# Performance work log

Measured on AMD Instinct MI355X. Metric: run time of the kernel, lower is better.

The kernel has to match this reference:

```python
import jax, jax.numpy as jnp
import numpy as np

B_SIZE, STEPS, UNITS = 128, 1024, 1024
E = 2 * STEPS              # model_internal_dim = expand_factor * model_input_dims
DT_RANK = (STEPS + 1) // 2 # math.ceil(model_input_dims / 2)
N = UNITS // 2             # model_states
COND = 512                 # conditioning feature size
K = 4                      # conv kernel size


def setup_inputs() -> dict:
    key = jax.random.key(0)
    ks = jax.random.split(key, 12)
    s = lambda k, shape, fan: jax.random.normal(k, shape, jnp.float32) / np.sqrt(fan)
    return {
        "x": jax.random.normal(ks[0], (B_SIZE, 1, STEPS), jnp.float32),
        "c": jax.random.normal(ks[1], (B_SIZE, COND), jnp.float32),
        "ln_g": jnp.ones((STEPS,), jnp.float32),
        "ln_b": jnp.zeros((STEPS,), jnp.float32),
        "W_in": s(ks[2], (STEPS, 2 * E), STEPS),
        "conv_w": s(ks[3], (K, 1, E), K),
        "conv_b": jnp.zeros((E,), jnp.float32),
        "W_x": s(ks[4], (E, DT_RANK + 2 * N), E),
        "W_dt": s(ks[5], (DT_RANK, E), DT_RANK),
        "b_dt": jnp.zeros((E,), jnp.float32),
        "A_log": jnp.log(jnp.tile(jnp.arange(1, N + 1, dtype=jnp.float32), (E, 1))),
        "D": jnp.ones((E,), jnp.float32),
        "W_out": s(ks[6], (E, STEPS), E),
        "b_out": jnp.zeros((STEPS,), jnp.float32),
        "W_d": s(ks[7], (STEPS, N), STEPS),
        "b_d": jnp.zeros((N,), jnp.float32),
        "W_f": s(ks[8], (COND, 2 * N), COND),
        "b_f": jnp.zeros((2 * N,), jnp.float32),
        "W_o": s(ks[9], (N, STEPS), N),
        "b_o": jnp.zeros((STEPS,), jnp.float32),
    }


def _selective_scan(u, delta, A, Bm, Cm, D):
    # u, delta: (b,l,e); A: (e,n); Bm, Cm: (b,l,n); D: (e,)
    dA = jnp.exp(jnp.einsum('ble,en->blen', delta, A))        # discretized A
    dBu = jnp.einsum('ble,ble,bln->blen', delta, u, Bm)       # discretized B*u

    def step(h, t):
        dA_t, dBu_t, C_t = t
        h = dA_t * h + dBu_t                                  # (b,e,n)
        return h, jnp.einsum('ben,bn->be', h, C_t)

    h0 = jnp.zeros((dA.shape[0], dA.shape[2], dA.shape[3]), dA.dtype)
    _, ys = jax.lax.scan(step, h0, (dA.transpose(1, 0, 2, 3),
                                    dBu.transpose(1, 0, 2, 3),
                                    Cm.transpose(1, 0, 2)))
    y = ys.transpose(1, 0, 2)                                 # (b,l,e)
    return y + u * D


def reference(x, c, ln_g, ln_b, W_in, conv_w, conv_b, W_x, W_dt, b_dt,
              A_log, D, W_out, b_out, W_d, b_d, W_f, b_f, W_o, b_o):
    # --- ResidualBlock: LayerNorm -> MambaBlock -> + x ---
    mu = jnp.mean(x, -1, keepdims=True)
    var = jnp.var(x, -1, keepdims=True)
    h = (x - mu) * jax.lax.rsqrt(var + 1e-5) * ln_g + ln_b
    xz = h @ W_in                                             # (b,l,2E)
    xi, res = jnp.split(xz, 2, axis=-1)
    xc = jax.lax.conv_general_dilated(
        xi, conv_w, window_strides=(1,), padding=[(K - 1, 0)],
        dimension_numbers=('NWC', 'WIO', 'NWC'), feature_group_count=E) + conv_b
    u = jax.nn.silu(xc)
    x_dbl = u @ W_x                                           # (b,l,dt_rank+2N)
    d_r, Bm, Cm = jnp.split(x_dbl, [DT_RANK, DT_RANK + N], axis=-1)
    delta = jax.nn.softplus(d_r @ W_dt + b_dt)                # (b,l,E)
    A = -jnp.exp(A_log)
    y = _selective_scan(u, delta, A, Bm, Cm, D)
    y = y * jax.nn.silu(res)                                  # gating branch
    mamba_out = y @ W_out + b_out + x                         # residual add
    # --- Dense(model_states, gelu) then squeeze seq dim ---
    z = jax.nn.gelu(mamba_out @ W_d + b_d, approximate=False)
    z = jnp.squeeze(z, axis=1)                                # (b, N)
    # --- FiLM conditioning ---
    gb = c @ W_f + b_f
    g, b = jnp.split(gb, 2, axis=-1)
    z = z * g + b
    # --- output projection back to steps ---
    return z @ W_o + b_o
```

## Files before the change

### kernel.cpp

```cpp
#include <hip/hip_runtime.h>
#include <math.h>

#define E_DIM 2048

typedef __attribute__((ext_vector_type(8))) short short8;
typedef __attribute__((ext_vector_type(4))) float floatx4;

__device__ __forceinline__ float siluf(float v) { return v / (1.f + expf(-v)); }

__device__ __forceinline__ short f2bf(float f) {
    unsigned u = __float_as_uint(f);
    u += 0x7fffu + ((u >> 16) & 1u);
    return (short)(u >> 16);
}

__global__ __launch_bounds__(256) void ln_cvt_kernel(const float* __restrict__ x,
                                                     const float* __restrict__ g,
                                                     const float* __restrict__ be,
                                                     const float* __restrict__ c,
                                                     short* __restrict__ h_bf,
                                                     short* __restrict__ c_bf) {
    int b = blockIdx.x;
    int tid = threadIdx.x;
    __shared__ float sdata[256];
    const float* xr = x + b * 1024;
    float v[4];
    float s = 0.f;
#pragma unroll
    for (int i = 0; i < 4; ++i) { v[i] = xr[tid + i * 256]; s += v[i]; }
    sdata[tid] = s; __syncthreads();
    for (int st = 128; st > 0; st >>= 1) { if (tid < st) sdata[tid] += sdata[tid + st]; __syncthreads(); }
    float mu = sdata[0] * (1.f / 1024.f);
    __syncthreads();
    float s2 = 0.f;
#pragma unroll
    for (int i = 0; i < 4; ++i) { float d = v[i] - mu; s2 += d * d; }
    sdata[tid] = s2; __syncthreads();
    for (int st = 128; st > 0; st >>= 1) { if (tid < st) sdata[tid] += sdata[tid + st]; __syncthreads(); }
    float var = sdata[0] * (1.f / 1024.f);
    float inv = rsqrtf(var + 1e-5f);
    short* hr = h_bf + b * 1024;
#pragma unroll
    for (int i = 0; i < 4; ++i) {
        int j = tid + i * 256;
        hr[j] = f2bf((v[i] - mu) * inv * g[j] + be[j]);
    }
    const float* cr = c + b * 512;
    short* cbr = c_bf + b * 512;
    for (int j = tid; j < 512; j += 256) cbr[j] = f2bf(cr[j]);
}

__global__ __launch_bounds__(256) void gemm_mfma(const short* __restrict__ A, int lda,
                                                 const float* __restrict__ B, int ldb,
                                                 float* __restrict__ C, int ldc,
                                                 int kChunk) {
    const int tid = threadIdx.x;
    const int w = tid >> 6;
    const int l = tid & 63;
    const int lane15 = l & 15;
    const int lgrp = l >> 4;
    const int n0 = blockIdx.x * 64;
    const int k0 = blockIdx.z * kChunk;

    const short* Ap0 = A + (w * 32 + lane15) * lda + lgrp * 8 + k0;
    const short* Ap1 = Ap0 + 16 * lda;
    const float* Bp = B + (size_t)(k0 + lgrp * 8) * ldb + n0 + lane15;

    floatx4 acc[2][4];
#pragma unroll
    for (int i = 0; i < 2; ++i)
#pragma unroll
        for (int j = 0; j < 4; ++j) acc[i][j] = (floatx4)0.f;

    for (int ks = 0; ks < kChunk; ks += 32) {
        short8 a0 = *(const short8*)(Ap0);
        short8 a1 = *(const short8*)(Ap1);
        Ap0 += 32; Ap1 += 32;
        float bv[4][8];
#pragma unroll
        for (int i = 0; i < 8; ++i) {
            const float* Br = Bp + i * ldb;
#pragma unroll
            for (int nt = 0; nt < 4; ++nt) bv[nt][i] = Br[nt * 16];
        }
        Bp += 32 * (size_t)ldb;
        short8 vb[4];
#pragma unroll
        for (int nt = 0; nt < 4; ++nt)
#pragma unroll
            for (int i = 0; i < 8; ++i) vb[nt][i] = f2bf(bv[nt][i]);
#pragma unroll
        for (int nt = 0; nt < 4; ++nt) {
            acc[0][nt] = __builtin_amdgcn_mfma_f32_16x16x32_bf16(a0, vb[nt], acc[0][nt], 0, 0, 0);
            acc[1][nt] = __builtin_amdgcn_mfma_f32_16x16x32_bf16(a1, vb[nt], acc[1][nt], 0, 0, 0);
        }
    }
    const int rbase = w * 32 + lgrp * 4;
#pragma unroll
    for (int mf = 0; mf < 2; ++mf)
#pragma unroll
        for (int nt = 0; nt < 4; ++nt)
#pragma unroll
            for (int r = 0; r < 4; ++r)
                atomicAdd(&C[(rbase + mf * 16 + r) * ldc + n0 + nt * 16 + lane15], acc[mf][nt][r]);
}

__global__ __launch_bounds__(256) void e1_kernel(const float* __restrict__ xz,
                                                 const float* __restrict__ convw,
                                                 const float* __restrict__ convb,
                                                 float* __restrict__ u_f32,
                                                 short* __restrict__ u_bf,
                                                 float* __restrict__ sres) {
    int idx = blockIdx.x * 256 + threadIdx.x;
    int b = idx >> 12, j = idx & 4095;
    float val = xz[idx];
    if (j < E_DIM) {
        float xc = val * convw[3 * E_DIM + j] + convb[j];
        float s = siluf(xc);
        u_f32[b * E_DIM + j] = s;
        u_bf[b * E_DIM + j] = f2bf(s);
    } else {
        sres[b * E_DIM + (j - E_DIM)] = siluf(val);
    }
}

__global__ __launch_bounds__(256) void svec_cvt_kernel(const float* __restrict__ xdbl,
                                                       float* __restrict__ svec,
                                                       short* __restrict__ dr_bf) {
    int b = blockIdx.x;
    int tid = threadIdx.x;
    __shared__ float sdata[256];
    const float* row = xdbl + b * 1536;
    float s = 0.f;
    for (int n = tid; n < 512; n += 256) s += row[512 + n] * row[1024 + n];
    sdata[tid] = s; __syncthreads();
    for (int st = 128; st > 0; st >>= 1) { if (tid < st) sdata[tid] += sdata[tid + st]; __syncthreads(); }
    if (tid == 0) svec[b] = sdata[0];
    short* dr = dr_bf + b * 512;
    for (int n = tid; n < 512; n += 256) dr[n] = f2bf(row[n]);
}

__global__ __launch_bounds__(256) void e3_kernel(const float* __restrict__ dacc,
                                                 const float* __restrict__ b_dt,
                                                 const float* __restrict__ u,
                                                 const float* __restrict__ sres,
                                                 const float* __restrict__ svec,
                                                 const float* __restrict__ Dv,
                                                 short* __restrict__ y_bf) {
    int idx = blockIdx.x * 256 + threadIdx.x;
    int b = idx >> 11, j = idx & 2047;
    float t = dacc[idx] + b_dt[j];
    float delta = fmaxf(t, 0.f) + log1pf(expf(-fabsf(t)));
    y_bf[idx] = f2bf(u[idx] * (delta * svec[b] + Dv[j]) * sres[idx]);
}

__global__ __launch_bounds__(256) void e4_kernel(const float* __restrict__ mo,
                                                 const float* __restrict__ b_out,
                                                 const float* __restrict__ x,
                                                 short* __restrict__ mamba_bf) {
    int idx = blockIdx.x * 256 + threadIdx.x;
    int j = idx & 1023;
    mamba_bf[idx] = f2bf(mo[idx] + b_out[j] + x[idx]);
}

__global__ __launch_bounds__(256) void e5_kernel(const float* __restrict__ zd,
                                                 const float* __restrict__ b_d,
                                                 const float* __restrict__ gb,
                                                 const float* __restrict__ b_f,
                                                 short* __restrict__ z_bf) {
    int idx = blockIdx.x * 256 + threadIdx.x;
    int b = idx >> 9, n = idx & 511;
    float t = zd[idx] + b_d[n];
    float zg = 0.5f * t * (1.f + erff(t * 0.70710678118654752f));
    float gq = gb[b * 1024 + n] + b_f[n];
    float bb = gb[b * 1024 + 512 + n] + b_f[512 + n];
    z_bf[idx] = f2bf(zg * gq + bb);
}

__global__ __launch_bounds__(256) void e6_kernel(const float* __restrict__ oa,
                                                 const float* __restrict__ b_o,
                                                 float* __restrict__ out) {
    int idx = blockIdx.x * 256 + threadIdx.x;
    int j = idx & 1023;
    out[idx] = oa[idx] + b_o[j];
}

extern "C" void kernel_launch(void* const* d_in, const int* in_sizes, int n_in,
                              void* d_out, int out_size, void* d_ws, size_t ws_size,
                              hipStream_t stream) {
    (void)in_sizes; (void)n_in; (void)out_size; (void)ws_size;
    const float* x     = (const float*)d_in[0];
    const float* c     = (const float*)d_in[1];
    const float* ln_g  = (const float*)d_in[2];
    const float* ln_b  = (const float*)d_in[3];
    const float* W_in  = (const float*)d_in[4];
    const float* convw = (const float*)d_in[5];
    const float* convb = (const float*)d_in[6];
    const float* W_x   = (const float*)d_in[7];
    const float* W_dt  = (const float*)d_in[8];
    const float* b_dt  = (const float*)d_in[9];
    const float* Dv    = (const float*)d_in[11];
    const float* W_out = (const float*)d_in[12];
    const float* b_out = (const float*)d_in[13];
    const float* W_d   = (const float*)d_in[14];
    const float* b_d   = (const float*)d_in[15];
    const float* W_f   = (const float*)d_in[16];
    const float* b_f   = (const float*)d_in[17];
    const float* W_o   = (const float*)d_in[18];
    const float* b_o   = (const float*)d_in[19];
    float* out = (float*)d_out;

    char* ws = (char*)d_ws;
    size_t off = 0;
    auto allocf = [&](size_t nElem) { float* p = (float*)(ws + off); off += nElem * sizeof(float); return p; };
    auto allocs = [&](size_t nElem) { short* p = (short*)(ws + off); off += nElem * sizeof(short); return p; };
    float* xz_acc   = allocf(128 * 4096);
    float* xdbl_acc = allocf(128 * 1536);
    float* dacc     = allocf(128 * 2048);
    float* mo_acc   = allocf(128 * 1024);
    float* zd_acc   = allocf(128 * 512);
    float* gb_acc   = allocf(128 * 1024);
    float* out_acc  = allocf(128 * 1024);
    size_t accBytes = off;
    float* u_f32  = allocf(128 * 2048);
    float* sres   = allocf(128 * 2048);
    float* svec   = allocf(128);
    short* h_bf   = allocs(128 * 1024);
    short* c_bf   = allocs(128 * 512);
    short* u_bf   = allocs(128 * 2048);
    short* dr_bf  = allocs(128 * 512);
    short* y_bf   = allocs(128 * 2048);
    short* mamba_bf = allocs(128 * 1024);
    short* z_bf   = allocs(128 * 512);

    hipMemsetAsync(d_ws, 0, accBytes, stream);

    ln_cvt_kernel<<<128, 256, 0, stream>>>(x, ln_g, ln_b, c, h_bf, c_bf);
    gemm_mfma<<<dim3(64, 1, 4), 256, 0, stream>>>(h_bf, 1024, W_in, 4096, xz_acc, 4096, 256);
    gemm_mfma<<<dim3(16, 1, 8), 256, 0, stream>>>(c_bf, 512, W_f, 1024, gb_acc, 1024, 64);
    e1_kernel<<<(128 * 4096) / 256, 256, 0, stream>>>(xz_acc, convw, convb, u_f32, u_bf, sres);
    gemm_mfma<<<dim3(24, 1, 8), 256, 0, stream>>>(u_bf, 2048, W_x, 1536, xdbl_acc, 1536, 256);
    svec_cvt_kernel<<<128, 256, 0, stream>>>(xdbl_acc, svec, dr_bf);
    gemm_mfma<<<dim3(32, 1, 8), 256, 0, stream>>>(dr_bf, 512, W_dt, 2048, dacc, 2048, 64);
    e3_kernel<<<(128 * 2048) / 256, 256, 0, stream>>>(dacc, b_dt, u_f32, sres, svec, Dv, y_bf);
    gemm_mfma<<<dim3(16, 1, 8), 256, 0, stream>>>(y_bf, 2048, W_out, 1024, mo_acc, 1024, 256);
    e4_kernel<<<(128 * 1024) / 256, 256, 0, stream>>>(mo_acc, b_out, x, mamba_bf);
    gemm_mfma<<<dim3(8, 1, 16), 256, 0, stream>>>(mamba_bf, 1024, W_d, 512, zd_acc, 512, 64);
    e5_kernel<<<(128 * 512) / 256, 256, 0, stream>>>(zd_acc, b_d, gb_acc, b_f, z_bf);
    gemm_mfma<<<dim3(16, 1, 8), 256, 0, stream>>>(z_bf, 512, W_o, 1024, out_acc, 1024, 64);
    e6_kernel<<<(128 * 1024) / 256, 256, 0, stream>>>(out_acc, b_o, out);
}
```

Baseline: 91.39 us.

## Fuse elementwise epilogues into GEMM A-loads and merge workspace zeroing into layernorm

Removes the separate elementwise kernels (conv+silu, dr conversion, residual add, gelu+FiLM) by templating the GEMM A-fragment load so it reads fp32 accumulators and applies the transform before converting to bf16. The svec reduction and the y computation are merged into one per-row kernel that recomputes u and silu(res) directly from xz. The hipMemsetAsync is replaced by extra blocks in the layernorm kernel that zero the accumulators. This cuts launches and intermediate buffers, but A-operand loads become scalar fp32 with repeated transcendental work, since every column block recomputes the same activations.

```diff
diff --git a/kernel.cpp b/kernel.cpp
--- a/kernel.cpp
+++ b/kernel.cpp
@@ -14,43 +14,97 @@
     return (short)(u >> 16);
 }
 
-__global__ __launch_bounds__(256) void ln_cvt_kernel(const float* __restrict__ x,
-                                                     const float* __restrict__ g,
-                                                     const float* __restrict__ be,
-                                                     const float* __restrict__ c,
-                                                     short* __restrict__ h_bf,
-                                                     short* __restrict__ c_bf) {
-    int b = blockIdx.x;
+__global__ __launch_bounds__(256) void ln_zero_kernel(const float* __restrict__ x,
+                                                      const float* __restrict__ g,
+                                                      const float* __restrict__ be,
+                                                      const float* __restrict__ c,
+                                                      short* __restrict__ h_bf,
+                                                      short* __restrict__ c_bf,
+                                                      float4* __restrict__ zbase,
+                                                      int zTotal) {
     int tid = threadIdx.x;
-    __shared__ float sdata[256];
-    const float* xr = x + b * 1024;
-    float v[4];
-    float s = 0.f;
-#pragma unroll
-    for (int i = 0; i < 4; ++i) { v[i] = xr[tid + i * 256]; s += v[i]; }
-    sdata[tid] = s; __syncthreads();
-    for (int st = 128; st > 0; st >>= 1) { if (tid < st) sdata[tid] += sdata[tid + st]; __syncthreads(); }
-    float mu = sdata[0] * (1.f / 1024.f);
-    __syncthreads();
-    float s2 = 0.f;
-#pragma unroll
-    for (int i = 0; i < 4; ++i) { float d = v[i] - mu; s2 += d * d; }
-    sdata[tid] = s2; __syncthreads();
-    for (int st = 128; st > 0; st >>= 1) { if (tid < st) sdata[tid] += sdata[tid + st]; __syncthreads(); }
-    float var = sdata[0] * (1.f / 1024.f);
-    float inv = rsqrtf(var + 1e-5f);
-    short* hr = h_bf + b * 1024;
-#pragma unroll
-    for (int i = 0; i < 4; ++i) {
-        int j = tid + i * 256;
-        hr[j] = f2bf((v[i] - mu) * inv * g[j] + be[j]);
-    }
-    const float* cr = c + b * 512;
-    short* cbr = c_bf + b * 512;
-    for (int j = tid; j < 512; j += 256) cbr[j] = f2bf(cr[j]);
-}
-
-__global__ __launch_bounds__(256) void gemm_mfma(const short* __restrict__ A, int lda,
+    if (blockIdx.x < 128) {
+        int b = blockIdx.x;
+        __shared__ float sdata[256];
+        const float* xr = x + b * 1024;
+        float v[4];
+        float s = 0.f;
+#pragma unroll
+        for (int i = 0; i < 4; ++i) { v[i] = xr[tid + i * 256]; s += v[i]; }
+        sdata[tid] = s; __syncthreads();
+        for (int st = 128; st > 0; st >>= 1) { if (tid < st) sdata[tid] += sdata[tid + st]; __syncthreads(); }
+        float mu = sdata[0] * (1.f / 1024.f);
+        __syncthreads();
+        float s2 = 0.f;
+#pragma unroll
+        for (int i = 0; i < 4; ++i) { float d = v[i] - mu; s2 += d * d; }
+        sdata[tid] = s2; __syncthreads();
+        for (int st = 128; st > 0; st >>= 1) { if (tid < st) sdata[tid] += sdata[tid + st]; __syncthreads(); }
+        float var = sdata[0] * (1.f / 1024.f);
+        float inv = rsqrtf(var + 1e-5f);
+        short* hr = h_bf + b * 1024;
+#pragma unroll
+        for (int i = 0; i < 4; ++i) {
+            int j = tid + i * 256;
+            hr[j] = f2bf((v[i] - mu) * inv * g[j] + be[j]);
+        }
+        const float* cr = c + b * 512;
+        short* cbr = c_bf + b * 512;
+        for (int j = tid; j < 512; j += 256) cbr[j] = f2bf(cr[j]);
+    } else {
+        int base = (blockIdx.x - 128) * 2048 + tid;
+        int stride = (gridDim.x - 128) * 2048;
+        for (int idx = base; idx < zTotal; idx += stride) {
+#pragma unroll
+            for (int i = 0; i < 8; ++i) {
+                int k = idx + i * 256;
+                if (k < zTotal) zbase[k] = (float4){0.f, 0.f, 0.f, 0.f};
+            }
+        }
+    }
+}
+
+template<int MODE>
+__device__ __forceinline__ short8 load_a_frag(const void* __restrict__ A, int lda, int r, int j0,
+                                              const float* __restrict__ aux0,
+                                              const float* __restrict__ aux1,
+                                              const float* __restrict__ aux2) {
+    if constexpr (MODE == 0) {
+        return *(const short8*)((const short*)A + (size_t)r * lda + j0);
+    } else {
+        const float* p = (const float*)A + (size_t)r * lda + j0;
+        float v[8];
+        if constexpr (MODE == 1) {
+#pragma unroll
+            for (int i = 0; i < 8; ++i) v[i] = siluf(p[i] * aux0[j0 + i] + aux1[j0 + i]);
+        } else if constexpr (MODE == 2) {
+#pragma unroll
+            for (int i = 0; i < 8; ++i) v[i] = p[i];
+        } else if constexpr (MODE == 3) {
+#pragma unroll
+            for (int i = 0; i < 8; ++i) v[i] = p[i] + aux0[j0 + i] + aux1[(size_t)r * lda + j0 + i];
+        } else {
+#pragma unroll
+            for (int i = 0; i < 8; ++i) {
+                float t = p[i] + aux0[j0 + i];
+                float zg = 0.5f * t * (1.f + erff(t * 0.70710678118654752f));
+                float gq = aux1[(size_t)r * 1024 + j0 + i] + aux2[j0 + i];
+                float bb = aux1[(size_t)r * 1024 + 512 + j0 + i] + aux2[512 + j0 + i];
+                v[i] = zg * gq + bb;
+            }
+        }
+        short8 s;
+#pragma unroll
+        for (int i = 0; i < 8; ++i) s[i] = f2bf(v[i]);
+        return s;
+    }
+}
+
+template<int MODE>
+__global__ __launch_bounds__(256) void gemm_mfma(const void* __restrict__ A, int lda,
+                                                 const float* __restrict__ aux0,
+                                                 const float* __restrict__ aux1,
+                                                 const float* __restrict__ aux2,
                                                  const float* __restrict__ B, int ldb,
                                                  float* __restrict__ C, int ldc,
                                                  int kChunk) {
@@ -62,8 +116,7 @@
     const int n0 = blockIdx.x * 64;
     const int k0 = blockIdx.z * kChunk;
 
-    const short* Ap0 = A + (w * 32 + lane15) * lda + lgrp * 8 + k0;
-    const short* Ap1 = Ap0 + 16 * lda;
+    const int r0 = w * 32 + lane15;
     const float* Bp = B + (size_t)(k0 + lgrp * 8) * ldb + n0 + lane15;
 
     floatx4 acc[2][4];
@@ -73,9 +126,9 @@
         for (int j = 0; j < 4; ++j) acc[i][j] = (floatx4)0.f;
 
     for (int ks = 0; ks < kChunk; ks += 32) {
-        short8 a0 = *(const short8*)(Ap0);
-        short8 a1 = *(const short8*)(Ap1);
-        Ap0 += 32; Ap1 += 32;
+        int j0 = k0 + ks + lgrp * 8;
+        short8 a0 = load_a_frag<MODE>(A, lda, r0, j0, aux0, aux1, aux2);
+        short8 a1 = load_a_frag<MODE>(A, lda, r0 + 16, j0, aux0, aux1, aux2);
         float bv[4][8];
 #pragma unroll
         for (int i = 0; i < 8; ++i) {
@@ -105,28 +158,14 @@
                 atomicAdd(&C[(rbase + mf * 16 + r) * ldc + n0 + nt * 16 + lane15], acc[mf][nt][r]);
 }
 
-__global__ __launch_bounds__(256) void e1_kernel(const float* __restrict__ xz,
-                                                 const float* __restrict__ convw,
+__global__ __launch_bounds__(256) void e3_kernel(const float* __restrict__ dacc,
+                                                 const float* __restrict__ b_dt,
+                                                 const float* __restrict__ xz,
+                                                 const float* __restrict__ convw3,
                                                  const float* __restrict__ convb,
-                                                 float* __restrict__ u_f32,
-                                                 short* __restrict__ u_bf,
-                                                 float* __restrict__ sres) {
-    int idx = blockIdx.x * 256 + threadIdx.x;
-    int b = idx >> 12, j = idx & 4095;
-    float val = xz[idx];
-    if (j < E_DIM) {
-        float xc = val * convw[3 * E_DIM + j] + convb[j];
-        float s = siluf(xc);
-        u_f32[b * E_DIM + j] = s;
-        u_bf[b * E_DIM + j] = f2bf(s);
-    } else {
-        sres[b * E_DIM + (j - E_DIM)] = siluf(val);
-    }
-}
-
-__global__ __launch_bounds__(256) void svec_cvt_kernel(const float* __restrict__ xdbl,
-                                                       float* __restrict__ svec,
-                                                       short* __restrict__ dr_bf) {
+                                                 const float* __restrict__ xdbl,
+                                                 const float* __restrict__ Dv,
+                                                 short* __restrict__ y_bf) {
     int b = blockIdx.x;
     int tid = threadIdx.x;
     __shared__ float sdata[256];
@@ -135,46 +174,19 @@
     for (int n = tid; n < 512; n += 256) s += row[512 + n] * row[1024 + n];
     sdata[tid] = s; __syncthreads();
     for (int st = 128; st > 0; st >>= 1) { if (tid < st) sdata[tid] += sdata[tid + st]; __syncthreads(); }
-    if (tid == 0) svec[b] = sdata[0];
-    short* dr = dr_bf + b * 512;
-    for (int n = tid; n < 512; n += 256) dr[n] = f2bf(row[n]);
-}
-
-__global__ __launch_bounds__(256) void e3_kernel(const float* __restrict__ dacc,
-                                                 const float* __restrict__ b_dt,
-                                                 const float* __restrict__ u,
-                                                 const float* __restrict__ sres,
-                                                 const float* __restrict__ svec,
-                                                 const float* __restrict__ Dv,
-                                                 short* __restrict__ y_bf) {
-    int idx = blockIdx.x * 256 + threadIdx.x;
-    int b = idx >> 11, j = idx & 2047;
-    float t = dacc[idx] + b_dt[j];
-    float delta = fmaxf(t, 0.f) + log1pf(expf(-fabsf(t)));
-    y_bf[idx] = f2bf(u[idx] * (delta * svec[b] + Dv[j]) * sres[idx]);
-}
-
-__global__ __launch_bounds__(256) void e4_kernel(const float* __restrict__ mo,
-                                                 const float* __restrict__ b_out,
-                                                 const float* __restrict__ x,
-                                                 short* __restrict__ mamba_bf) {
-    int idx = blockIdx.x * 256 + threadIdx.x;
-    int j = idx & 1023;
-    mamba_bf[idx] = f2bf(mo[idx] + b_out[j] + x[idx]);
-}
-
-__global__ __launch_bounds__(256) void e5_kernel(const float* __restrict__ zd,
-                                                 const float* __restrict__ b_d,
-                                                 const float* __restrict__ gb,
-                                                 const float* __restrict__ b_f,
-                                                 short* __restrict__ z_bf) {
-    int idx = blockIdx.x * 256 + threadIdx.x;
-    int b = idx >> 9, n = idx & 511;
-    float t = zd[idx] + b_d[n];
-    float zg = 0.5f * t * (1.f + erff(t * 0.70710678118654752f));
-    float gq = gb[b * 1024 + n] + b_f[n];
-    float bb = gb[b * 1024 + 512 + n] + b_f[512 + n];
-    z_bf[idx] = f2bf(zg * gq + bb);
+    float svec = sdata[0];
+    const float* xzr = xz + b * 4096;
+    const float* dar = dacc + b * 2048;
+    short* yr = y_bf + b * 2048;
+#pragma unroll
+    for (int ii = 0; ii < 8; ++ii) {
+        int j = tid + ii * 256;
+        float t = dar[j] + b_dt[j];
+        float delta = fmaxf(t, 0.f) + log1pf(expf(-fabsf(t)));
+        float u = siluf(xzr[j] * convw3[j] + convb[j]);
+        float sr = siluf(xzr[2048 + j]);
+        yr[j] = f2bf(u * (delta * svec + Dv[j]) * sr);
+    }
 }
 
 __global__ __launch_bounds__(256) void e6_kernel(const float* __restrict__ oa,
@@ -222,31 +234,28 @@
     float* gb_acc   = allocf(128 * 1024);
     float* out_acc  = allocf(128 * 1024);
     size_t accBytes = off;
-    float* u_f32  = allocf(128 * 2048);
-    float* sres   = allocf(128 * 2048);
-    float* svec   = allocf(128);
+    int zTotal = (int)(accBytes / 16);
     short* h_bf   = allocs(128 * 1024);
     short* c_bf   = allocs(128 * 512);
-    short* u_bf   = allocs(128 * 2048);
-    short* dr_bf  = allocs(128 * 512);
     short* y_bf   = allocs(128 * 2048);
-    short* mamba_bf = allocs(128 * 1024);
-    short* z_bf   = allocs(128 * 512);
-
-    hipMemsetAsync(d_ws, 0, accBytes, stream);
-
-    ln_cvt_kernel<<<128, 256, 0, stream>>>(x, ln_g, ln_b, c, h_bf, c_bf);
-    gemm_mfma<<<dim3(64, 1, 4), 256, 0, stream>>>(h_bf, 1024, W_in, 4096, xz_acc, 4096, 256);
-    gemm_mfma<<<dim3(16, 1, 8), 256, 0, stream>>>(c_bf, 512, W_f, 1024, gb_acc, 1024, 64);
-    e1_kernel<<<(128 * 4096) / 256, 256, 0, stream>>>(xz_acc, convw, convb, u_f32, u_bf, sres);
-    gemm_mfma<<<dim3(24, 1, 8), 256, 0, stream>>>(u_bf, 2048, W_x, 1536, xdbl_acc, 1536, 256);
-    svec_cvt_kernel<<<128, 256, 0, stream>>>(xdbl_acc, svec, dr_bf);
-    gemm_mfma<<<dim3(32, 1, 8), 256, 0, stream>>>(dr_bf, 512, W_dt, 2048, dacc, 2048, 64);
-    e3_kernel<<<(128 * 2048) / 256, 256, 0, stream>>>(dacc, b_dt, u_f32, sres, svec, Dv, y_bf);
-    gemm_mfma<<<dim3(16, 1, 8), 256, 0, stream>>>(y_bf, 2048, W_out, 1024, mo_acc, 1024, 256);
-    e4_kernel<<<(128 * 1024) / 256, 256, 0, stream>>>(mo_acc, b_out, x, mamba_bf);
-    gemm_mfma<<<dim3(8, 1, 16), 256, 0, stream>>>(mamba_bf, 1024, W_d, 512, zd_acc, 512, 64);
-    e5_kernel<<<(128 * 512) / 256, 256, 0, stream>>>(zd_acc, b_d, gb_acc, b_f, z_bf);
-    gemm_mfma<<<dim3(16, 1, 8), 256, 0, stream>>>(z_bf, 512, W_o, 1024, out_acc, 1024, 64);
+
+    ln_zero_kernel<<<128 + 176, 256, 0, stream>>>(x, ln_g, ln_b, c, h_bf, c_bf,
+                                                  (float4*)d_ws, zTotal);
+    gemm_mfma<0><<<dim3(64, 1, 4), 256, 0, stream>>>(h_bf, 1024, nullptr, nullptr, nullptr,
+                                                     W_in, 4096, xz_acc, 4096, 256);
+    gemm_mfma<0><<<dim3(16, 1, 8), 256, 0, stream>>>(c_bf, 512, nullptr, nullptr, nullptr,
+                                                     W_f, 1024, gb_acc, 1024, 64);
+    gemm_mfma<1><<<dim3(24, 1, 8), 256, 0, stream>>>(xz_acc, 4096, convw + 3 * E_DIM, convb, nullptr,
+                                                     W_x, 1536, xdbl_acc, 1536, 256);
+    gemm_mfma<2><<<dim3(32, 1, 8), 256, 0, stream>>>(xdbl_acc, 1536, nullptr, nullptr, nullptr,
+                                                     W_dt, 2048, dacc, 2048, 64);
+    e3_kernel<<<128, 256, 0, stream>>>(dacc, b_dt, xz_acc, convw + 3 * E_DIM, convb,
+                                       xdbl_acc, Dv, y_bf);
+    gemm_mfma<0><<<dim3(16, 1, 8), 256, 0, stream>>>(y_bf, 2048, nullptr, nullptr, nullptr,
+                                                     W_out, 1024, mo_acc, 1024, 256);
+    gemm_mfma<3><<<dim3(8, 1, 16), 256, 0, stream>>>(mo_acc, 1024, b_out, x, nullptr,
+                                                     W_d, 512, zd_acc, 512, 64);
+    gemm_mfma<4><<<dim3(16, 1, 8), 256, 0, stream>>>(zd_acc, 512, b_d, gb_acc, b_f,
+                                                     W_o, 1024, out_acc, 1024, 64);
     e6_kernel<<<(128 * 1024) / 256, 256, 0, stream>>>(out_acc, b_o, out);
 }
```

Result: slower. 103.9 us (+13.7%).

## Replace atomic split-K accumulation with per-slice partial buffers and fuse reductions

Applied to the files above, without the earlier changes.

Each split-K GEMM now writes plain stores into its own slice buffer instead of atomically adding into a zeroed accumulator. The following elementwise kernels sum the slices, which removes both the workspace memset and the atomic traffic. The e4 kernel is folded into the W_d GEMM, whose A-operand loader sums the W_out partials, bias and residual on the fly. Split factors are retuned per GEMM. The cost is more workspace memory and extra partial-buffer reads in consumers, and the fused loader repeats the A-side summation across column blocks.

```diff
diff --git a/kernel.cpp b/kernel.cpp
--- a/kernel.cpp
+++ b/kernel.cpp
@@ -50,10 +50,13 @@
     for (int j = tid; j < 512; j += 256) cbr[j] = f2bf(cr[j]);
 }
 
-__global__ __launch_bounds__(256) void gemm_mfma(const short* __restrict__ A, int lda,
-                                                 const float* __restrict__ B, int ldb,
-                                                 float* __restrict__ C, int ldc,
-                                                 int kChunk) {
+template<int MODE, int S_A>
+__global__ __launch_bounds__(256) void gemm_k(const void* __restrict__ A, int lda,
+                                              const float* __restrict__ aux0,
+                                              const float* __restrict__ aux1,
+                                              const float* __restrict__ B, int ldb,
+                                              float* __restrict__ Cp, int ldc,
+                                              int kChunk) {
     const int tid = threadIdx.x;
     const int w = tid >> 6;
     const int l = tid & 63;
@@ -62,8 +65,7 @@
     const int n0 = blockIdx.x * 64;
     const int k0 = blockIdx.z * kChunk;
 
-    const short* Ap0 = A + (w * 32 + lane15) * lda + lgrp * 8 + k0;
-    const short* Ap1 = Ap0 + 16 * lda;
+    const int r0 = w * 32 + lane15;
     const float* Bp = B + (size_t)(k0 + lgrp * 8) * ldb + n0 + lane15;
 
     floatx4 acc[2][4];
@@ -73,9 +75,31 @@
         for (int j = 0; j < 4; ++j) acc[i][j] = (floatx4)0.f;
 
     for (int ks = 0; ks < kChunk; ks += 32) {
-        short8 a0 = *(const short8*)(Ap0);
-        short8 a1 = *(const short8*)(Ap1);
-        Ap0 += 32; Ap1 += 32;
+        int j0 = k0 + ks + lgrp * 8;
+        short8 a0, a1;
+        if constexpr (MODE == 0) {
+            a0 = *(const short8*)((const short*)A + (size_t)r0 * lda + j0);
+            a1 = *(const short8*)((const short*)A + (size_t)(r0 + 16) * lda + j0);
+        } else {
+            const float* Af = (const float*)A;
+#pragma unroll
+            for (int rr = 0; rr < 2; ++rr) {
+                int r = r0 + rr * 16;
+                float v[8];
+#pragma unroll
+                for (int i = 0; i < 8; ++i) {
+                    float t = aux0[j0 + i] + aux1[(size_t)r * lda + j0 + i];
+#pragma unroll
+                    for (int s = 0; s < S_A; ++s)
+                        t += Af[(size_t)s * 128 * 1024 + (size_t)r * lda + j0 + i];
+                    v[i] = t;
+                }
+                short8 sv;
+#pragma unroll
+                for (int i = 0; i < 8; ++i) sv[i] = f2bf(v[i]);
+                if (rr == 0) a0 = sv; else a1 = sv;
+            }
+        }
         float bv[4][8];
 #pragma unroll
         for (int i = 0; i < 8; ++i) {
@@ -95,6 +119,7 @@
             acc[1][nt] = __builtin_amdgcn_mfma_f32_16x16x32_bf16(a1, vb[nt], acc[1][nt], 0, 0, 0);
         }
     }
+    float* Cs = Cp + (size_t)blockIdx.z * 128 * ldc;
     const int rbase = w * 32 + lgrp * 4;
 #pragma unroll
     for (int mf = 0; mf < 2; ++mf)
@@ -102,20 +127,20 @@
         for (int nt = 0; nt < 4; ++nt)
 #pragma unroll
             for (int r = 0; r < 4; ++r)
-                atomicAdd(&C[(rbase + mf * 16 + r) * ldc + n0 + nt * 16 + lane15], acc[mf][nt][r]);
-}
-
-__global__ __launch_bounds__(256) void e1_kernel(const float* __restrict__ xz,
-                                                 const float* __restrict__ convw,
+                Cs[(size_t)(rbase + mf * 16 + r) * ldc + n0 + nt * 16 + lane15] = acc[mf][nt][r];
+}
+
+__global__ __launch_bounds__(256) void e1_kernel(const float* __restrict__ xz_p,
+                                                 const float* __restrict__ convw3,
                                                  const float* __restrict__ convb,
                                                  float* __restrict__ u_f32,
                                                  short* __restrict__ u_bf,
                                                  float* __restrict__ sres) {
     int idx = blockIdx.x * 256 + threadIdx.x;
     int b = idx >> 12, j = idx & 4095;
-    float val = xz[idx];
+    float val = xz_p[idx] + xz_p[128 * 4096 + idx];
     if (j < E_DIM) {
-        float xc = val * convw[3 * E_DIM + j] + convb[j];
+        float xc = val * convw3[j] + convb[j];
         float s = siluf(xc);
         u_f32[b * E_DIM + j] = s;
         u_bf[b * E_DIM + j] = f2bf(s);
@@ -124,23 +149,34 @@
     }
 }
 
-__global__ __launch_bounds__(256) void svec_cvt_kernel(const float* __restrict__ xdbl,
+__global__ __launch_bounds__(256) void svec_cvt_kernel(const float* __restrict__ xdbl_p,
                                                        float* __restrict__ svec,
                                                        short* __restrict__ dr_bf) {
     int b = blockIdx.x;
     int tid = threadIdx.x;
     __shared__ float sdata[256];
-    const float* row = xdbl + b * 1536;
+    const float* row = xdbl_p + (size_t)b * 1536;
+    const size_t SL = (size_t)128 * 1536;
     float s = 0.f;
-    for (int n = tid; n < 512; n += 256) s += row[512 + n] * row[1024 + n];
+    for (int n = tid; n < 512; n += 256) {
+        float bm = 0.f, cm = 0.f;
+#pragma unroll
+        for (int k = 0; k < 8; ++k) { bm += row[k * SL + 512 + n]; cm += row[k * SL + 1024 + n]; }
+        s += bm * cm;
+    }
     sdata[tid] = s; __syncthreads();
     for (int st = 128; st > 0; st >>= 1) { if (tid < st) sdata[tid] += sdata[tid + st]; __syncthreads(); }
     if (tid == 0) svec[b] = sdata[0];
     short* dr = dr_bf + b * 512;
-    for (int n = tid; n < 512; n += 256) dr[n] = f2bf(row[n]);
-}
-
-__global__ __launch_bounds__(256) void e3_kernel(const float* __restrict__ dacc,
+    for (int n = tid; n < 512; n += 256) {
+        float t = 0.f;
+#pragma unroll
+        for (int k = 0; k < 8; ++k) t += row[k * SL + n];
+        dr[n] = f2bf(t);
+    }
+}
+
+__global__ __launch_bounds__(256) void e3_kernel(const float* __restrict__ dacc_p,
                                                  const float* __restrict__ b_dt,
                                                  const float* __restrict__ u,
                                                  const float* __restrict__ sres,
@@ -149,40 +185,42 @@
                                                  short* __restrict__ y_bf) {
     int idx = blockIdx.x * 256 + threadIdx.x;
     int b = idx >> 11, j = idx & 2047;
-    float t = dacc[idx] + b_dt[j];
+    float t = b_dt[j];
+#pragma unroll
+    for (int s = 0; s < 8; ++s) t += dacc_p[(size_t)s * 128 * 2048 + idx];
     float delta = fmaxf(t, 0.f) + log1pf(expf(-fabsf(t)));
     y_bf[idx] = f2bf(u[idx] * (delta * svec[b] + Dv[j]) * sres[idx]);
 }
 
-__global__ __launch_bounds__(256) void e4_kernel(const float* __restrict__ mo,
-                                                 const float* __restrict__ b_out,
-                                                 const float* __restrict__ x,
-                                                 short* __restrict__ mamba_bf) {
-    int idx = blockIdx.x * 256 + threadIdx.x;
-    int j = idx & 1023;
-    mamba_bf[idx] = f2bf(mo[idx] + b_out[j] + x[idx]);
-}
-
-__global__ __launch_bounds__(256) void e5_kernel(const float* __restrict__ zd,
+__global__ __launch_bounds__(256) void e5_kernel(const float* __restrict__ zd_p,
                                                  const float* __restrict__ b_d,
-                                                 const float* __restrict__ gb,
+                                                 const float* __restrict__ gb_p,
                                                  const float* __restrict__ b_f,
                                                  short* __restrict__ z_bf) {
     int idx = blockIdx.x * 256 + threadIdx.x;
     int b = idx >> 9, n = idx & 511;
-    float t = zd[idx] + b_d[n];
+    float t = b_d[n];
+#pragma unroll
+    for (int s = 0; s < 8; ++s) t += zd_p[(size_t)s * 128 * 512 + idx];
     float zg = 0.5f * t * (1.f + erff(t * 0.70710678118654752f));
-    float gq = gb[b * 1024 + n] + b_f[n];
-    float bb = gb[b * 1024 + 512 + n] + b_f[512 + n];
+    float gq = b_f[n], bb = b_f[512 + n];
+#pragma unroll
+    for (int s = 0; s < 2; ++s) {
+        gq += gb_p[(size_t)s * 128 * 1024 + b * 1024 + n];
+        bb += gb_p[(size_t)s * 128 * 1024 + b * 1024 + 512 + n];
+    }
     z_bf[idx] = f2bf(zg * gq + bb);
 }
 
-__global__ __launch_bounds__(256) void e6_kernel(const float* __restrict__ oa,
+__global__ __launch_bounds__(256) void e6_kernel(const float* __restrict__ out_p,
                                                  const float* __restrict__ b_o,
                                                  float* __restrict__ out) {
     int idx = blockIdx.x * 256 + threadIdx.x;
     int j = idx & 1023;
-    out[idx] = oa[idx] + b_o[j];
+    float t = b_o[j];
+#pragma unroll
+    for (int s = 0; s < 4; ++s) t += out_p[(size_t)s * 128 * 1024 + idx];
+    out[idx] = t;
 }
 
 extern "C" void kernel_launch(void* const* d_in, const int* in_sizes, int n_in,
@@ -214,14 +252,13 @@
     size_t off = 0;
     auto allocf = [&](size_t nElem) { float* p = (float*)(ws + off); off += nElem * sizeof(float); return p; };
     auto allocs = [&](size_t nElem) { short* p = (short*)(ws + off); off += nElem * sizeof(short); return p; };
-    float* xz_acc   = allocf(128 * 4096);
-    float* xdbl_acc = allocf(128 * 1536);
-    float* dacc     = allocf(128 * 2048);
-    float* mo_acc   = allocf(128 * 1024);
-    float* zd_acc   = allocf(128 * 512);
-    float* gb_acc   = allocf(128 * 1024);
-    float* out_acc  = allocf(128 * 1024);
-    size_t accBytes = off;
+    float* xz_p   = allocf(2 * 128 * 4096);
+    float* gb_p   = allocf(2 * 128 * 1024);
+    float* xdbl_p = allocf(8 * 128 * 1536);
+    float* dacc_p = allocf(8 * 128 * 2048);
+    float* mo_p   = allocf(4 * 128 * 1024);
+    float* zd_p   = allocf(8 * 128 * 512);
+    float* out_p  = allocf(4 * 128 * 1024);
     float* u_f32  = allocf(128 * 2048);
     float* sres   = allocf(128 * 2048);
     float* svec   = allocf(128);
@@ -230,23 +267,27 @@
     short* u_bf   = allocs(128 * 2048);
     short* dr_bf  = allocs(128 * 512);
     short* y_bf   = allocs(128 * 2048);
-    short* mamba_bf = allocs(128 * 1024);
     short* z_bf   = allocs(128 * 512);
 
-    hipMemsetAsync(d_ws, 0, accBytes, stream);
-
     ln_cvt_kernel<<<128, 256, 0, stream>>>(x, ln_g, ln_b, c, h_bf, c_bf);
-    gemm_mfma<<<dim3(64, 1, 4), 256, 0, stream>>>(h_bf, 1024, W_in, 4096, xz_acc, 4096, 256);
-    gemm_mfma<<<dim3(16, 1, 8), 256, 0, stream>>>(c_bf, 512, W_f, 1024, gb_acc, 1024, 64);
-    e1_kernel<<<(128 * 4096) / 256, 256, 0, stream>>>(xz_acc, convw, convb, u_f32, u_bf, sres);
-    gemm_mfma<<<dim3(24, 1, 8), 256, 0, stream>>>(u_bf, 2048, W_x, 1536, xdbl_acc, 1536, 256);
-    svec_cvt_kernel<<<128, 256, 0, stream>>>(xdbl_acc, svec, dr_bf);
-    gemm_mfma<<<dim3(32, 1, 8), 256, 0, stream>>>(dr_bf, 512, W_dt, 2048, dacc, 2048, 64);
-    e3_kernel<<<(128 * 2048) / 256, 256, 0, stream>>>(dacc, b_dt, u_f32, sres, svec, Dv, y_bf);
-    gemm_mfma<<<dim3(16, 1, 8), 256, 0, stream>>>(y_bf, 2048, W_out, 1024, mo_acc, 1024, 256);
-    e4_kernel<<<(128 * 1024) / 256, 256, 0, stream>>>(mo_acc, b_out, x, mamba_bf);
-    gemm_mfma<<<dim3(8, 1, 16), 256, 0, stream>>>(mamba_bf, 1024, W_d, 512, zd_acc, 512, 64);
-    e5_kernel<<<(128 * 512) / 256, 256, 0, stream>>>(zd_acc, b_d, gb_acc, b_f, z_bf);
-    gemm_mfma<<<dim3(16, 1, 8), 256, 0, stream>>>(z_bf, 512, W_o, 1024, out_acc, 1024, 64);
-    e6_kernel<<<(128 * 1024) / 256, 256, 0, stream>>>(out_acc, b_o, out);
-}
+    gemm_k<0, 0><<<dim3(64, 1, 2), 256, 0, stream>>>(h_bf, 1024, nullptr, nullptr,
+                                                     W_in, 4096, xz_p, 4096, 512);
+    gemm_k<0, 0><<<dim3(16, 1, 2), 256, 0, stream>>>(c_bf, 512, nullptr, nullptr,
+                                                     W_f, 1024, gb_p, 1024, 256);
+    e1_kernel<<<(128 * 4096) / 256, 256, 0, stream>>>(xz_p, convw + 3 * E_DIM, convb,
+                                                      u_f32, u_bf, sres);
+    gemm_k<0, 0><<<dim3(24, 1, 8), 256, 0, stream>>>(u_bf, 2048, nullptr, nullptr,
+                                                     W_x, 1536, xdbl_p, 1536, 256);
+    svec_cvt_kernel<<<128, 256, 0, stream>>>(xdbl_p, svec, dr_bf);
+    gemm_k<0, 0><<<dim3(32, 1, 8), 256, 0, stream>>>(dr_bf, 512, nullptr, nullptr,
+                                                     W_dt, 2048, dacc_p, 2048, 64);
+    e3_kernel<<<(128 * 2048) / 256, 256, 0, stream>>>(dacc_p, b_dt, u_f32, sres, svec, Dv, y_bf);
+    gemm_k<0, 0><<<dim3(16, 1, 4), 256, 0, stream>>>(y_bf, 2048, nullptr, nullptr,
+                                                     W_out, 1024, mo_p, 1024, 512);
+    gemm_k<3, 4><<<dim3(8, 1, 8), 256, 0, stream>>>(mo_p, 1024, b_out, x,
+                                                    W_d, 512, zd_p, 512, 128);
+    e5_kernel<<<(128 * 512) / 256, 256, 0, stream>>>(zd_p, b_d, gb_p, b_f, z_bf);
+    gemm_k<0, 0><<<dim3(16, 1, 4), 256, 0, stream>>>(z_bf, 512, nullptr, nullptr,
+                                                     W_o, 1024, out_p, 1024, 128);
+    e6_kernel<<<(128 * 1024) / 256, 256, 0, stream>>>(out_p, b_o, out);
+}
```

New measurement: 97.37 us. +6.5%, slower.

## Fuse elementwise epilogues into GEMMs and drop split-K atomics

Applied to the files above, without the earlier changes.

Replaces the split-K atomic GEMM plus separate elementwise kernels with per-layer GEMM kernels that compute the full K reduction in one block (128 rows × 32 columns, 8 waves) and apply the activation, bias and gating epilogue directly. This removes the workspace memset, the atomic traffic and several launches and intermediate round-trips. It also fuses the W_in and W_f GEMMs into a single launch and adds register double-buffering of the next A/B loads. The trade is far fewer blocks (16 to 160) with long serial K loops, so on a chip with many CUs occupancy is low and each block must stream the whole weight slice alone.

```diff
diff --git a/kernel.cpp b/kernel.cpp
--- a/kernel.cpp
+++ b/kernel.cpp
@@ -1,7 +1,5 @@
 #include <hip/hip_runtime.h>
 #include <math.h>
-
-#define E_DIM 2048
 
 typedef __attribute__((ext_vector_type(8))) short short8;
 typedef __attribute__((ext_vector_type(4))) float floatx4;
@@ -37,8 +35,7 @@
     for (int i = 0; i < 4; ++i) { float d = v[i] - mu; s2 += d * d; }
     sdata[tid] = s2; __syncthreads();
     for (int st = 128; st > 0; st >>= 1) { if (tid < st) sdata[tid] += sdata[tid + st]; __syncthreads(); }
-    float var = sdata[0] * (1.f / 1024.f);
-    float inv = rsqrtf(var + 1e-5f);
+    float inv = rsqrtf(sdata[0] * (1.f / 1024.f) + 1e-5f);
     short* hr = h_bf + b * 1024;
 #pragma unroll
     for (int i = 0; i < 4; ++i) {
@@ -47,142 +44,232 @@
     }
     const float* cr = c + b * 512;
     short* cbr = c_bf + b * 512;
-    for (int j = tid; j < 512; j += 256) cbr[j] = f2bf(cr[j]);
-}
-
-__global__ __launch_bounds__(256) void gemm_mfma(const short* __restrict__ A, int lda,
-                                                 const float* __restrict__ B, int ldb,
-                                                 float* __restrict__ C, int ldc,
-                                                 int kChunk) {
+    cbr[tid] = f2bf(cr[tid]);
+    cbr[tid + 256] = f2bf(cr[tid + 256]);
+}
+
+template<int KSTEPS>
+__device__ __forceinline__ void gemm32(const short* __restrict__ A, int lda,
+                                       const float* __restrict__ B, int ldb,
+                                       int n0, floatx4 acc[2]) {
     const int tid = threadIdx.x;
     const int w = tid >> 6;
     const int l = tid & 63;
     const int lane15 = l & 15;
     const int lgrp = l >> 4;
-    const int n0 = blockIdx.x * 64;
-    const int k0 = blockIdx.z * kChunk;
-
-    const short* Ap0 = A + (w * 32 + lane15) * lda + lgrp * 8 + k0;
-    const short* Ap1 = Ap0 + 16 * lda;
-    const float* Bp = B + (size_t)(k0 + lgrp * 8) * ldb + n0 + lane15;
-
-    floatx4 acc[2][4];
-#pragma unroll
-    for (int i = 0; i < 2; ++i)
-#pragma unroll
-        for (int j = 0; j < 4; ++j) acc[i][j] = (floatx4)0.f;
-
-    for (int ks = 0; ks < kChunk; ks += 32) {
-        short8 a0 = *(const short8*)(Ap0);
-        short8 a1 = *(const short8*)(Ap1);
-        Ap0 += 32; Ap1 += 32;
-        float bv[4][8];
-#pragma unroll
-        for (int i = 0; i < 8; ++i) {
-            const float* Br = Bp + i * ldb;
-#pragma unroll
-            for (int nt = 0; nt < 4; ++nt) bv[nt][i] = Br[nt * 16];
-        }
-        Bp += 32 * (size_t)ldb;
-        short8 vb[4];
-#pragma unroll
-        for (int nt = 0; nt < 4; ++nt)
-#pragma unroll
-            for (int i = 0; i < 8; ++i) vb[nt][i] = f2bf(bv[nt][i]);
-#pragma unroll
-        for (int nt = 0; nt < 4; ++nt) {
-            acc[0][nt] = __builtin_amdgcn_mfma_f32_16x16x32_bf16(a0, vb[nt], acc[0][nt], 0, 0, 0);
-            acc[1][nt] = __builtin_amdgcn_mfma_f32_16x16x32_bf16(a1, vb[nt], acc[1][nt], 0, 0, 0);
-        }
-    }
-    const int rbase = w * 32 + lgrp * 4;
-#pragma unroll
-    for (int mf = 0; mf < 2; ++mf)
-#pragma unroll
-        for (int nt = 0; nt < 4; ++nt)
+    const int r0 = w * 16 + lane15;
+    const short* Ap = A + (size_t)r0 * lda + lgrp * 8;
+    const float* Bp = B + (size_t)(lgrp * 8) * ldb + n0 + lane15;
+    acc[0] = (floatx4)0.f;
+    acc[1] = (floatx4)0.f;
+
+    short8 a_cur = *(const short8*)Ap; Ap += 32;
+    float bv_cur[2][8];
+#pragma unroll
+    for (int i = 0; i < 8; ++i) {
+        const float* Br = Bp + (size_t)i * ldb;
+        bv_cur[0][i] = Br[0];
+        bv_cur[1][i] = Br[16];
+    }
+    Bp += 32 * (size_t)ldb;
+
+#pragma unroll
+    for (int s = 0; s < KSTEPS; ++s) {
+        short8 a_nxt;
+        float bv_nxt[2][8];
+        if (s + 1 < KSTEPS) {
+            a_nxt = *(const short8*)Ap; Ap += 32;
+#pragma unroll
+            for (int i = 0; i < 8; ++i) {
+                const float* Br = Bp + (size_t)i * ldb;
+                bv_nxt[0][i] = Br[0];
+                bv_nxt[1][i] = Br[16];
+            }
+            Bp += 32 * (size_t)ldb;
+        }
+        short8 vb0, vb1;
+#pragma unroll
+        for (int i = 0; i < 8; ++i) { vb0[i] = f2bf(bv_cur[0][i]); vb1[i] = f2bf(bv_cur[1][i]); }
+        acc[0] = __builtin_amdgcn_mfma_f32_16x16x32_bf16(a_cur, vb0, acc[0], 0, 0, 0);
+        acc[1] = __builtin_amdgcn_mfma_f32_16x16x32_bf16(a_cur, vb1, acc[1], 0, 0, 0);
+        a_cur = a_nxt;
+#pragma unroll
+        for (int i = 0; i < 8; ++i) { bv_cur[0][i] = bv_nxt[0][i]; bv_cur[1][i] = bv_nxt[1][i]; }
+    }
+}
+
+#define EPI_SETUP \
+    const int tid = threadIdx.x; \
+    const int lane15 = tid & 15; \
+    const int rbase = (tid >> 6) * 16 + ((tid & 63) >> 4) * 4;
+
+__global__ __launch_bounds__(512) void g1g6_kernel(const short* __restrict__ h_bf,
+                                                   const float* __restrict__ W_in,
+                                                   const short* __restrict__ c_bf,
+                                                   const float* __restrict__ W_f,
+                                                   const float* __restrict__ cw3,
+                                                   const float* __restrict__ cb,
+                                                   float* __restrict__ u_f32,
+                                                   short* __restrict__ u_bf,
+                                                   float* __restrict__ sres,
+                                                   float* __restrict__ gb) {
+    EPI_SETUP
+    floatx4 acc[2];
+    if (blockIdx.x < 128) {
+        int n0 = blockIdx.x * 32;
+        gemm32<32>(h_bf, 1024, W_in, 4096, n0, acc);
+#pragma unroll
+        for (int nt = 0; nt < 2; ++nt) {
+            int col = n0 + nt * 16 + lane15;
+#pragma unroll
+            for (int r = 0; r < 4; ++r) {
+                int row = rbase + r;
+                float val = acc[nt][r];
+                if (col < 2048) {
+                    float u = siluf(val * cw3[col] + cb[col]);
+                    u_f32[(size_t)row * 2048 + col] = u;
+                    u_bf[(size_t)row * 2048 + col] = f2bf(u);
+                } else {
+                    sres[(size_t)row * 2048 + col - 2048] = siluf(val);
+                }
+            }
+        }
+    } else {
+        int n0 = (blockIdx.x - 128) * 32;
+        gemm32<16>(c_bf, 512, W_f, 1024, n0, acc);
+#pragma unroll
+        for (int nt = 0; nt < 2; ++nt) {
+            int col = n0 + nt * 16 + lane15;
 #pragma unroll
             for (int r = 0; r < 4; ++r)
-                atomicAdd(&C[(rbase + mf * 16 + r) * ldc + n0 + nt * 16 + lane15], acc[mf][nt][r]);
-}
-
-__global__ __launch_bounds__(256) void e1_kernel(const float* __restrict__ xz,
-                                                 const float* __restrict__ convw,
-                                                 const float* __restrict__ convb,
-                                                 float* __restrict__ u_f32,
-                                                 short* __restrict__ u_bf,
-                                                 float* __restrict__ sres) {
-    int idx = blockIdx.x * 256 + threadIdx.x;
-    int b = idx >> 12, j = idx & 4095;
-    float val = xz[idx];
-    if (j < E_DIM) {
-        float xc = val * convw[3 * E_DIM + j] + convb[j];
-        float s = siluf(xc);
-        u_f32[b * E_DIM + j] = s;
-        u_bf[b * E_DIM + j] = f2bf(s);
-    } else {
-        sres[b * E_DIM + (j - E_DIM)] = siluf(val);
-    }
-}
-
-__global__ __launch_bounds__(256) void svec_cvt_kernel(const float* __restrict__ xdbl,
-                                                       float* __restrict__ svec,
-                                                       short* __restrict__ dr_bf) {
+                gb[(size_t)(rbase + r) * 1024 + col] = acc[nt][r];
+        }
+    }
+}
+
+__global__ __launch_bounds__(512) void g2_kernel(const short* __restrict__ u_bf,
+                                                 const float* __restrict__ W_x,
+                                                 short* __restrict__ dr_bf,
+                                                 float* __restrict__ bc) {
+    EPI_SETUP
+    floatx4 acc[2];
+    int n0 = blockIdx.x * 32;
+    gemm32<64>(u_bf, 2048, W_x, 1536, n0, acc);
+#pragma unroll
+    for (int nt = 0; nt < 2; ++nt) {
+        int col = n0 + nt * 16 + lane15;
+#pragma unroll
+        for (int r = 0; r < 4; ++r) {
+            int row = rbase + r;
+            float val = acc[nt][r];
+            if (col < 512) dr_bf[(size_t)row * 512 + col] = f2bf(val);
+            else           bc[(size_t)row * 1024 + col - 512] = val;
+        }
+    }
+}
+
+__global__ __launch_bounds__(256) void svec_kernel(const float* __restrict__ bc,
+                                                   float* __restrict__ svec) {
     int b = blockIdx.x;
     int tid = threadIdx.x;
     __shared__ float sdata[256];
-    const float* row = xdbl + b * 1536;
-    float s = 0.f;
-    for (int n = tid; n < 512; n += 256) s += row[512 + n] * row[1024 + n];
+    const float* row = bc + (size_t)b * 1024;
+    float s = row[tid] * row[512 + tid];
+    int t2 = tid + 256;
+    if (t2 < 512) {}
+    s += row[tid + 256] * row[768 + tid];
     sdata[tid] = s; __syncthreads();
     for (int st = 128; st > 0; st >>= 1) { if (tid < st) sdata[tid] += sdata[tid + st]; __syncthreads(); }
     if (tid == 0) svec[b] = sdata[0];
-    short* dr = dr_bf + b * 512;
-    for (int n = tid; n < 512; n += 256) dr[n] = f2bf(row[n]);
-}
-
-__global__ __launch_bounds__(256) void e3_kernel(const float* __restrict__ dacc,
+}
+
+__global__ __launch_bounds__(512) void g3_kernel(const short* __restrict__ dr_bf,
+                                                 const float* __restrict__ W_dt,
                                                  const float* __restrict__ b_dt,
-                                                 const float* __restrict__ u,
-                                                 const float* __restrict__ sres,
                                                  const float* __restrict__ svec,
                                                  const float* __restrict__ Dv,
+                                                 const float* __restrict__ u_f32,
+                                                 const float* __restrict__ sres,
                                                  short* __restrict__ y_bf) {
-    int idx = blockIdx.x * 256 + threadIdx.x;
-    int b = idx >> 11, j = idx & 2047;
-    float t = dacc[idx] + b_dt[j];
-    float delta = fmaxf(t, 0.f) + log1pf(expf(-fabsf(t)));
-    y_bf[idx] = f2bf(u[idx] * (delta * svec[b] + Dv[j]) * sres[idx]);
-}
-
-__global__ __launch_bounds__(256) void e4_kernel(const float* __restrict__ mo,
+    EPI_SETUP
+    floatx4 acc[2];
+    int n0 = blockIdx.x * 32;
+    gemm32<16>(dr_bf, 512, W_dt, 2048, n0, acc);
+#pragma unroll
+    for (int nt = 0; nt < 2; ++nt) {
+        int col = n0 + nt * 16 + lane15;
+#pragma unroll
+        for (int r = 0; r < 4; ++r) {
+            int row = rbase + r;
+            float t = acc[nt][r] + b_dt[col];
+            float delta = fmaxf(t, 0.f) + log1pf(expf(-fabsf(t)));
+            size_t idx = (size_t)row * 2048 + col;
+            y_bf[idx] = f2bf(u_f32[idx] * (delta * svec[row] + Dv[col]) * sres[idx]);
+        }
+    }
+}
+
+__global__ __launch_bounds__(512) void g4_kernel(const short* __restrict__ y_bf,
+                                                 const float* __restrict__ W_out,
                                                  const float* __restrict__ b_out,
                                                  const float* __restrict__ x,
                                                  short* __restrict__ mamba_bf) {
-    int idx = blockIdx.x * 256 + threadIdx.x;
-    int j = idx & 1023;
-    mamba_bf[idx] = f2bf(mo[idx] + b_out[j] + x[idx]);
-}
-
-__global__ __launch_bounds__(256) void e5_kernel(const float* __restrict__ zd,
+    EPI_SETUP
+    floatx4 acc[2];
+    int n0 = blockIdx.x * 32;
+    gemm32<64>(y_bf, 2048, W_out, 1024, n0, acc);
+#pragma unroll
+    for (int nt = 0; nt < 2; ++nt) {
+        int col = n0 + nt * 16 + lane15;
+#pragma unroll
+        for (int r = 0; r < 4; ++r) {
+            int row = rbase + r;
+            size_t idx = (size_t)row * 1024 + col;
+            mamba_bf[idx] = f2bf(acc[nt][r] + b_out[col] + x[idx]);
+        }
+    }
+}
+
+__global__ __launch_bounds__(512) void g5_kernel(const short* __restrict__ mamba_bf,
+                                                 const float* __restrict__ W_d,
                                                  const float* __restrict__ b_d,
                                                  const float* __restrict__ gb,
                                                  const float* __restrict__ b_f,
                                                  short* __restrict__ z_bf) {
-    int idx = blockIdx.x * 256 + threadIdx.x;
-    int b = idx >> 9, n = idx & 511;
-    float t = zd[idx] + b_d[n];
-    float zg = 0.5f * t * (1.f + erff(t * 0.70710678118654752f));
-    float gq = gb[b * 1024 + n] + b_f[n];
-    float bb = gb[b * 1024 + 512 + n] + b_f[512 + n];
-    z_bf[idx] = f2bf(zg * gq + bb);
-}
-
-__global__ __launch_bounds__(256) void e6_kernel(const float* __restrict__ oa,
+    EPI_SETUP
+    floatx4 acc[2];
+    int n0 = blockIdx.x * 32;
+    gemm32<32>(mamba_bf, 1024, W_d, 512, n0, acc);
+#pragma unroll
+    for (int nt = 0; nt < 2; ++nt) {
+        int col = n0 + nt * 16 + lane15;
+#pragma unroll
+        for (int r = 0; r < 4; ++r) {
+            int row = rbase + r;
+            float t = acc[nt][r] + b_d[col];
+            float zg = 0.5f * t * (1.f + erff(t * 0.70710678118654752f));
+            float gq = gb[(size_t)row * 1024 + col] + b_f[col];
+            float bb = gb[(size_t)row * 1024 + 512 + col] + b_f[512 + col];
+            z_bf[(size_t)row * 512 + col] = f2bf(zg * gq + bb);
+        }
+    }
+}
+
+__global__ __launch_bounds__(512) void g7_kernel(const short* __restrict__ z_bf,
+                                                 const float* __restrict__ W_o,
                                                  const float* __restrict__ b_o,
                                                  float* __restrict__ out) {
-    int idx = blockIdx.x * 256 + threadIdx.x;
-    int j = idx & 1023;
-    out[idx] = oa[idx] + b_o[j];
+    EPI_SETUP
+    floatx4 acc[2];
+    int n0 = blockIdx.x * 32;
+    gemm32<16>(z_bf, 512, W_o, 1024, n0, acc);
+#pragma unroll
+    for (int nt = 0; nt < 2; ++nt) {
+        int col = n0 + nt * 16 + lane15;
+#pragma unroll
+        for (int r = 0; r < 4; ++r)
+            out[(size_t)(rbase + r) * 1024 + col] = acc[nt][r] + b_o[col];
+    }
 }
 
 extern "C" void kernel_launch(void* const* d_in, const int* in_sizes, int n_in,
@@ -212,41 +299,27 @@
 
     char* ws = (char*)d_ws;
     size_t off = 0;
-    auto allocf = [&](size_t nElem) { float* p = (float*)(ws + off); off += nElem * sizeof(float); return p; };
-    auto allocs = [&](size_t nElem) { short* p = (short*)(ws + off); off += nElem * sizeof(short); return p; };
-    float* xz_acc   = allocf(128 * 4096);
-    float* xdbl_acc = allocf(128 * 1536);
-    float* dacc     = allocf(128 * 2048);
-    float* mo_acc   = allocf(128 * 1024);
-    float* zd_acc   = allocf(128 * 512);
-    float* gb_acc   = allocf(128 * 1024);
-    float* out_acc  = allocf(128 * 1024);
-    size_t accBytes = off;
-    float* u_f32  = allocf(128 * 2048);
-    float* sres   = allocf(128 * 2048);
-    float* svec   = allocf(128);
-    short* h_bf   = allocs(128 * 1024);
-    short* c_bf   = allocs(128 * 512);
-    short* u_bf   = allocs(128 * 2048);
-    short* dr_bf  = allocs(128 * 512);
-    short* y_bf   = allocs(128 * 2048);
-    short* mamba_bf = allocs(128 * 1024);
-    short* z_bf   = allocs(128 * 512);
-
-    hipMemsetAsync(d_ws, 0, accBytes, stream);
+    auto alloc = [&](size_t bytes) { void* p = ws + off; off += (bytes + 255) & ~(size_t)255; return p; };
+    short* h_bf     = (short*)alloc(128 * 1024 * 2);
+    short* c_bf     = (short*)alloc(128 * 512 * 2);
+    float* u_f32    = (float*)alloc((size_t)128 * 2048 * 4);
+    short* u_bf     = (short*)alloc(128 * 2048 * 2);
+    float* sres     = (float*)alloc((size_t)128 * 2048 * 4);
+    float* gb       = (float*)alloc((size_t)128 * 1024 * 4);
+    short* dr_bf    = (short*)alloc(128 * 512 * 2);
+    float* bc       = (float*)alloc((size_t)128 * 1024 * 4);
+    float* svec     = (float*)alloc(128 * 4);
+    short* y_bf     = (short*)alloc(128 * 2048 * 2);
+    short* mamba_bf = (short*)alloc(128 * 1024 * 2);
+    short* z_bf     = (short*)alloc(128 * 512 * 2);
 
     ln_cvt_kernel<<<128, 256, 0, stream>>>(x, ln_g, ln_b, c, h_bf, c_bf);
-    gemm_mfma<<<dim3(64, 1, 4), 256, 0, stream>>>(h_bf, 1024, W_in, 4096, xz_acc, 4096, 256);
-    gemm_mfma<<<dim3(16, 1, 8), 256, 0, stream>>>(c_bf, 512, W_f, 1024, gb_acc, 1024, 64);
-    e1_kernel<<<(128 * 4096) / 256, 256, 0, stream>>>(xz_acc, convw, convb, u_f32, u_bf, sres);
-    gemm_mfma<<<dim3(24, 1, 8), 256, 0, stream>>>(u_bf, 2048, W_x, 1536, xdbl_acc, 1536, 256);
-    svec_cvt_kernel<<<128, 256, 0, stream>>>(xdbl_acc, svec, dr_bf);
-    gemm_mfma<<<dim3(32, 1, 8), 256, 0, stream>>>(dr_bf, 512, W_dt, 2048, dacc, 2048, 64);
-    e3_kernel<<<(128 * 2048) / 256, 256, 0, stream>>>(dacc, b_dt, u_f32, sres, svec, Dv, y_bf);
-    gemm_mfma<<<dim3(16, 1, 8), 256, 0, stream>>>(y_bf, 2048, W_out, 1024, mo_acc, 1024, 256);
-    e4_kernel<<<(128 * 1024) / 256, 256, 0, stream>>>(mo_acc, b_out, x, mamba_bf);
-    gemm_mfma<<<dim3(8, 1, 16), 256, 0, stream>>>(mamba_bf, 1024, W_d, 512, zd_acc, 512, 64);
-    e5_kernel<<<(128 * 512) / 256, 256, 0, stream>>>(zd_acc, b_d, gb_acc, b_f, z_bf);
-    gemm_mfma<<<dim3(16, 1, 8), 256, 0, stream>>>(z_bf, 512, W_o, 1024, out_acc, 1024, 64);
-    e6_kernel<<<(128 * 1024) / 256, 256, 0, stream>>>(out_acc, b_o, out);
-}
+    g1g6_kernel<<<160, 512, 0, stream>>>(h_bf, W_in, c_bf, W_f, convw + 3 * 2048, convb,
+                                         u_f32, u_bf, sres, gb);
+    g2_kernel<<<48, 512, 0, stream>>>(u_bf, W_x, dr_bf, bc);
+    svec_kernel<<<128, 256, 0, stream>>>(bc, svec);
+    g3_kernel<<<64, 512, 0, stream>>>(dr_bf, W_dt, b_dt, svec, Dv, u_f32, sres, y_bf);
+    g4_kernel<<<32, 512, 0, stream>>>(y_bf, W_out, b_out, x, mamba_bf);
+    g5_kernel<<<16, 512, 0, stream>>>(mamba_bf, W_d, b_d, gb, b_f, z_bf);
+    g7_kernel<<<32, 512, 0, stream>>>(z_bf, W_o, b_o, out);
+}
```

After: 143.0 us. +56.5%, slower.
